# Kernel tuning notes

Measured on AMD Instinct MI355X. Metric: run time of the kernel, lower is better.

## Reference

```python
import jax, jax.numpy as jnp
import numpy as np

B, C, O, K, H, W = 32, 256, 256, 7, 31, 31


def _unfold(x, k):
    """Extract kxk sliding windows (stride 1, no padding, no dilation).

    x: [B, C, H, W] -> patches [B, C, k, k, Ho, Wo]
    """
    _, _, h, w = x.shape
    ho, wo = h - k + 1, w - k + 1
    # fixed small loop over k*k window offsets (k=7 -> 49 cheap slices)
    rows = []
    for i in range(k):
        cols = [x[:, :, i:i + ho, j:j + wo] for j in range(k)]
        rows.append(jnp.stack(cols, axis=2))  # [B, C, k, Ho, Wo]
    return jnp.stack(rows, axis=2)  # [B, C, k, k, Ho, Wo]


def setup_inputs() -> dict:
    key = jax.random.key(0)
    k1, k2, k3, k4 = jax.random.split(key, 4)
    x = jax.random.normal(k1, (B, C, H, W), dtype=jnp.float32)
    kernel = jax.random.normal(k2, (B, C, K, K), dtype=jnp.float32)
    weight = jax.random.normal(k3, (O, C, K, K), dtype=jnp.float32) * 0.02
    bias = jax.random.normal(k4, (O,), dtype=jnp.float32) * 0.02
    return {"x": x, "kernel": kernel, "weight": weight, "bias": bias}


def reference(x, kernel, weight, bias):
    k = weight.shape[-1]
    patches = _unfold(x, k)  # [B, C, k, k, Ho, Wo]
    # fused: (patches * kernel[..., None, None]) contracted with weight
    # torch: einsum('ijklmn,ojkl->iomn', patches * kernel_view, weight)
    out = jnp.einsum('bcklhw,bckl,ockl->bohw', patches, kernel, weight)
    out = out + bias[None, :, None, None]
    return out
```

## Files before the change

### kernel.cpp

```cpp
#include <hip/hip_runtime.h>
#include <hip/hip_bf16.h>

typedef __attribute__((ext_vector_type(8)))  short short8;
typedef __attribute__((ext_vector_type(4)))  float floatx4;
typedef __attribute__((ext_vector_type(16))) float floatx16;

#define BB 32
#define CC 256
#define OO 256
#define KS 7
#define HH 31
#define WW 31
#define HO 25
#define PP 625
#define SS 49

#define SLAB_PITCH 40
#define SLAB_ROWS  310

#define WT4_ELEMS  ((size_t)SS * 8 * 2 * CC * 16)
#define WT4_BYTES  (WT4_ELEMS * 2)
#define KERNF_BYTES ((size_t)BB * SS * CC * 4)
#define WMOD_ELEMS ((size_t)BB * WT4_ELEMS)
#define WMOD_BYTES (WMOD_ELEMS * 2)

static __device__ __forceinline__ unsigned pk2(float lo, float hi) {
    float2 f; f.x = lo; f.y = hi;
    __hip_bfloat162 h = __float22bfloat162_rn(f);
    unsigned r;
    __builtin_memcpy(&r, &h, sizeof(r));
    return r;
}
static __device__ __forceinline__ float bflo(unsigned u) {
    return __builtin_bit_cast(float, u << 16);
}
static __device__ __forceinline__ float bfhi(unsigned u) {
    return __builtin_bit_cast(float, u & 0xffff0000u);
}

static __device__ __forceinline__ uint4 modpack(uint4 wv, float4 k0, float4 k1) {
    float p0 = bflo(wv.x) * k0.x, p1 = bfhi(wv.x) * k0.y;
    float p2 = bflo(wv.y) * k0.z, p3 = bfhi(wv.y) * k0.w;
    float p4 = bflo(wv.z) * k1.x, p5 = bfhi(wv.z) * k1.y;
    float p6 = bflo(wv.w) * k1.z, p7 = bfhi(wv.w) * k1.w;
    uint4 r;
    r.x = pk2(p0, p1); r.y = pk2(p2, p3); r.z = pk2(p4, p5); r.w = pk2(p6, p7);
    return r;
}

__global__ __launch_bounds__(256) void repack_w(const float* __restrict__ w,
                                                unsigned short* __restrict__ wt4) {
    const int bid = blockIdx.x;
    const int s = bid >> 3, cb = bid & 7;
    const int o = threadIdx.x;
    const float* src = w + ((size_t)o * CC + cb * 32) * SS + s;
    float v[32];
#pragma unroll
    for (int ci = 0; ci < 32; ++ci) v[ci] = src[(size_t)ci * SS];
#pragma unroll
    for (int kh = 0; kh < 2; ++kh) {
        unsigned short* dst = wt4 + ((size_t)bid * 2 + kh) * (CC * 16) + o * 16;
        uint4 p0, p1;
        p0.x = pk2(v[kh*16+0], v[kh*16+1]);  p0.y = pk2(v[kh*16+2], v[kh*16+3]);
        p0.z = pk2(v[kh*16+4], v[kh*16+5]);  p0.w = pk2(v[kh*16+6], v[kh*16+7]);
        p1.x = pk2(v[kh*16+8], v[kh*16+9]);  p1.y = pk2(v[kh*16+10], v[kh*16+11]);
        p1.z = pk2(v[kh*16+12], v[kh*16+13]); p1.w = pk2(v[kh*16+14], v[kh*16+15]);
        *(uint4*)(dst)     = p0;
        *(uint4*)(dst + 8) = p1;
    }
}

__global__ __launch_bounds__(256) void repack_k(const float* __restrict__ kern,
                                                float* __restrict__ kernf) {
    const int bid = blockIdx.x;
    const int b = bid / KS, kk = bid % KS;
    const int c = threadIdx.x;
    const float* src = kern + ((size_t)b * CC + c) * SS + kk * KS;
#pragma unroll
    for (int ll = 0; ll < KS; ++ll)
        kernf[((size_t)b * SS + kk * KS + ll) * CC + c] = src[ll];
}

__global__ __launch_bounds__(256) void premod(
        const unsigned short* __restrict__ wt4, const float* __restrict__ kern,
        unsigned short* __restrict__ wmod) {
    const int bid = blockIdx.x;
    const int b = bid / 392, rc = bid % 392;
    const int s = rc >> 3, cb = rc & 7;
    const int o = threadIdx.x;
    const float* kp = kern + ((size_t)b * CC + cb * 32) * SS + s;
    float kf[32];
#pragma unroll
    for (int ci = 0; ci < 32; ++ci) kf[ci] = kp[(size_t)ci * SS];
#pragma unroll
    for (int kh = 0; kh < 2; ++kh) {
        const size_t off = ((size_t)rc * 2 + kh) * (CC * 16) + o * 16;
        uint4 w0 = *(const uint4*)(wt4 + off);
        uint4 w1 = *(const uint4*)(wt4 + off + 8);
        float4 k0a, k0b, k1a, k1b;
        k0a.x = kf[kh*16+0];  k0a.y = kf[kh*16+1];  k0a.z = kf[kh*16+2];  k0a.w = kf[kh*16+3];
        k0b.x = kf[kh*16+4];  k0b.y = kf[kh*16+5];  k0b.z = kf[kh*16+6];  k0b.w = kf[kh*16+7];
        k1a.x = kf[kh*16+8];  k1a.y = kf[kh*16+9];  k1a.z = kf[kh*16+10]; k1a.w = kf[kh*16+11];
        k1b.x = kf[kh*16+12]; k1b.y = kf[kh*16+13]; k1b.z = kf[kh*16+14]; k1b.w = kf[kh*16+15];
        uint4 m0 = modpack(w0, k0a, k0b);
        uint4 m1 = modpack(w1, k1a, k1b);
        unsigned short* dst = wmod + (size_t)b * WT4_ELEMS + off;
        *(uint4*)(dst)     = m0;
        *(uint4*)(dst + 8) = m1;
    }
}

__global__ __launch_bounds__(256, 4) void dwconv_big(
        const float* __restrict__ x, const unsigned short* __restrict__ wmod,
        const float* __restrict__ bias, float* __restrict__ out) {
    __shared__ unsigned short slab[SLAB_ROWS * SLAB_PITCH];

    const int tid = threadIdx.x;
    const int id = blockIdx.x;
    const int hi = id / 80, rem = id % 80;
    const int px = rem >> 3;
    const int g = hi * 8 + (rem & 7);
    const int b = g >> 2, oy = g & 3;

    const int p0 = px * 64, o0 = oy * 64;
    const int h0 = p0 / HO;
    const int pmax = (p0 + 63 < PP - 1) ? p0 + 63 : PP - 1;
    const int rows = pmax / HO - h0 + 7;
    const int npos = rows * WW;

    const int lane = tid & 63, kw = tid >> 6;
    const int l32 = lane & 31, half = lane >> 5;

    int bOff[2];
#pragma unroll
    for (int ph = 0; ph < 2; ++ph) {
        int p = p0 + ph * 32 + l32;
        if (p > PP - 1) p = PP - 1;
        int h = p / HO, ww_ = p - h * HO;
        bOff[ph] = ((h - h0) * WW + ww_) * SLAB_PITCH + half * 8;
    }

    const int s0 = kw * 12 + (kw > 0 ? 1 : 0);
    const int ns = kw ? 12 : 13;

    const unsigned short* wmodb = wmod + (size_t)b * WT4_ELEMS
                                  + (size_t)(o0 + l32) * 16 + half * 8;

    floatx16 acc[2][2];
#pragma unroll
    for (int oh = 0; oh < 2; ++oh)
#pragma unroll
        for (int ph = 0; ph < 2; ++ph)
#pragma unroll
            for (int r = 0; r < 16; ++r) acc[oh][ph][r] = 0.f;

    for (int cb = 0; cb < 8; ++cb) {
        __syncthreads();
        {
            const float* xsrc = x + ((size_t)(b * CC + cb * 32 + kw * 8)) * (HH * WW)
                                  + h0 * WW;
#pragma unroll
            for (int it = 0; it < 5; ++it) {
                int pos = lane + it * 64;
                if (pos < npos) {
                    float v[8];
#pragma unroll
                    for (int j = 0; j < 8; ++j) v[j] = xsrc[j * (HH * WW) + pos];
                    uint4 pkt;
                    pkt.x = pk2(v[0], v[1]); pkt.y = pk2(v[2], v[3]);
                    pkt.z = pk2(v[4], v[5]); pkt.w = pk2(v[6], v[7]);
                    *(uint4*)(slab + pos * SLAB_PITCH + kw * 8) = pkt;
                }
            }
        }
        __syncthreads();

        const unsigned short* aptr = wmodb + (size_t)(s0 * 8 + cb) * 8192;

        uint4 wa0 = *(const uint4*)(aptr);
        uint4 wa1 = *(const uint4*)(aptr + 512);
        uint4 wa2 = *(const uint4*)(aptr + 4096);
        uint4 wa3 = *(const uint4*)(aptr + 4096 + 512);

        int s = s0, kk = s0 / KS, ll = s0 - (s0 / KS) * KS;
        for (int si = 0; si < ns; ++si) {
            uint4 wn0, wn1, wn2, wn3;
            if (si + 1 < ns) {
                aptr += 65536;
                wn0 = *(const uint4*)(aptr);
                wn1 = *(const uint4*)(aptr + 512);
                wn2 = *(const uint4*)(aptr + 4096);
                wn3 = *(const uint4*)(aptr + 4096 + 512);
            } else {
                wn0 = wa0; wn1 = wa1; wn2 = wa2; wn3 = wa3;
            }

            const unsigned short* slabS = slab + (kk * WW + ll) * SLAB_PITCH;
            short8 sb00 = *(const short8*)(slabS + bOff[0]);
            short8 sb01 = *(const short8*)(slabS + bOff[0] + 16);
            short8 sb10 = *(const short8*)(slabS + bOff[1]);
            short8 sb11 = *(const short8*)(slabS + bOff[1] + 16);

            short8 a00 = __builtin_bit_cast(short8, wa0);
            short8 a10 = __builtin_bit_cast(short8, wa1);
            short8 a01 = __builtin_bit_cast(short8, wa2);
            short8 a11 = __builtin_bit_cast(short8, wa3);

            acc[0][0] = __builtin_amdgcn_mfma_f32_32x32x16_bf16(a00, sb00, acc[0][0], 0, 0, 0);
            acc[0][1] = __builtin_amdgcn_mfma_f32_32x32x16_bf16(a00, sb10, acc[0][1], 0, 0, 0);
            acc[1][0] = __builtin_amdgcn_mfma_f32_32x32x16_bf16(a10, sb00, acc[1][0], 0, 0, 0);
            acc[1][1] = __builtin_amdgcn_mfma_f32_32x32x16_bf16(a10, sb10, acc[1][1], 0, 0, 0);
            acc[0][0] = __builtin_amdgcn_mfma_f32_32x32x16_bf16(a01, sb01, acc[0][0], 0, 0, 0);
            acc[0][1] = __builtin_amdgcn_mfma_f32_32x32x16_bf16(a01, sb11, acc[0][1], 0, 0, 0);
            acc[1][0] = __builtin_amdgcn_mfma_f32_32x32x16_bf16(a11, sb01, acc[1][0], 0, 0, 0);
            acc[1][1] = __builtin_amdgcn_mfma_f32_32x32x16_bf16(a11, sb11, acc[1][1], 0, 0, 0);

            wa0 = wn0; wa1 = wn1; wa2 = wn2; wa3 = wn3;
            ++s; if (++ll == KS) { ll = 0; ++kk; }
        }
    }

    float* red = (float*)slab;
    __syncthreads();
    if (kw == 3) {
#pragma unroll
        for (int oh = 0; oh < 2; ++oh)
#pragma unroll
            for (int ph = 0; ph < 2; ++ph)
#pragma unroll
                for (int c = 0; c < 4; ++c) {
                    floatx4 v4 = {acc[oh][ph][4*c+0], acc[oh][ph][4*c+1],
                                  acc[oh][ph][4*c+2], acc[oh][ph][4*c+3]};
                    *(floatx4*)(red + (ph * 32 + l32) * 68 + oh * 32 + c * 8 + 4 * half) = v4;
                }
    }
    __syncthreads();
    if (kw == 2) {
#pragma unroll
        for (int oh = 0; oh < 2; ++oh)
#pragma unroll
            for (int ph = 0; ph < 2; ++ph)
#pragma unroll
                for (int c = 0; c < 4; ++c) {
                    float* rp = red + (ph * 32 + l32) * 68 + oh * 32 + c * 8 + 4 * half;
                    floatx4 v4 = *(floatx4*)rp;
                    v4[0] += acc[oh][ph][4*c+0]; v4[1] += acc[oh][ph][4*c+1];
                    v4[2] += acc[oh][ph][4*c+2]; v4[3] += acc[oh][ph][4*c+3];
                    *(floatx4*)rp = v4;
                }
    }
    __syncthreads();
    if (kw == 1) {
#pragma unroll
        for (int oh = 0; oh < 2; ++oh)
#pragma unroll
            for (int ph = 0; ph < 2; ++ph)
#pragma unroll
                for (int c = 0; c < 4; ++c) {
                    float* rp = red + (ph * 32 + l32) * 68 + oh * 32 + c * 8 + 4 * half;
                    floatx4 v4 = *(floatx4*)rp;
                    v4[0] += acc[oh][ph][4*c+0]; v4[1] += acc[oh][ph][4*c+1];
                    v4[2] += acc[oh][ph][4*c+2]; v4[3] += acc[oh][ph][4*c+3];
                    *(floatx4*)rp = v4;
                }
    }
    __syncthreads();
    if (kw == 0) {
#pragma unroll
        for (int oh = 0; oh < 2; ++oh)
#pragma unroll
            for (int c = 0; c < 4; ++c) {
                const int ob = o0 + oh * 32 + c * 8 + 4 * half;
                const float4 bv = *(const float4*)(bias + ob);
#pragma unroll
                for (int ph = 0; ph < 2; ++ph) {
                    const int p = p0 + ph * 32 + l32;
                    floatx4 v4 = *(floatx4*)(red + (ph * 32 + l32) * 68 + oh * 32 + c * 8 + 4 * half);
                    if (p < PP) {
                        out[((size_t)(b * OO + ob + 0)) * PP + p] = v4[0] + acc[oh][ph][4*c+0] + bv.x;
                        out[((size_t)(b * OO + ob + 1)) * PP + p] = v4[1] + acc[oh][ph][4*c+1] + bv.y;
                        out[((size_t)(b * OO + ob + 2)) * PP + p] = v4[2] + acc[oh][ph][4*c+2] + bv.z;
                        out[((size_t)(b * OO + ob + 3)) * PP + p] = v4[3] + acc[oh][ph][4*c+3] + bv.w;
                    }
                }
            }
    }
}

#define SLAB2_ROWS 372
__global__ __launch_bounds__(256, 3) void dwconv_mid(
        const float* __restrict__ x,
        const unsigned short* __restrict__ wt4, const float* __restrict__ kernf,
        const float* __restrict__ bias, float* __restrict__ out) {
    __shared__ unsigned short slab[SLAB2_ROWS * SLAB_PITCH];

    const int tid = threadIdx.x;
    const int id = blockIdx.x;
    const int oy = id & 3;
    const int t  = id >> 2;
    const int px = t % 5, b = t / 5;
    const int p0 = px * 128, o0 = oy * 64;
    const int h0 = p0 / HO;
    const int rows = (HH - h0) < 12 ? (HH - h0) : 12;
    const int npos = rows * WW;

    const int lane = tid & 63, wid = tid >> 6;
    const int pw = wid & 1, kw = wid >> 1;
    const int lo16 = lane & 15, quad = lane >> 4;

    int bOff[4];
#pragma unroll
    for (int pt = 0; pt < 4; ++pt) {
        int p = p0 + pw * 64 + pt * 16 + lo16;
        if (p > PP - 1) p = PP - 1;
        int h = p / HO, ww_ = p - h * HO;
        bOff[pt] = ((h - h0) * WW + ww_) * SLAB_PITCH + quad * 8;
    }

    const int s0 = kw ? 25 : 0;
    const int ns = kw ? 24 : 25;

    floatx4 acc[4][4];
#pragma unroll
    for (int at = 0; at < 4; ++at)
#pragma unroll
        for (int pt = 0; pt < 4; ++pt)
            acc[at][pt] = (floatx4){0.f, 0.f, 0.f, 0.f};

    for (int cb = 0; cb < 8; ++cb) {
        __syncthreads();
        {
            const int coct = wid;
            const float* xsrc = x + ((size_t)(b * CC + cb * 32 + coct * 8)) * (HH * WW)
                                  + h0 * WW;
#pragma unroll
            for (int it = 0; it < 6; ++it) {
                int pos = lane + it * 64;
                if (pos < npos) {
                    float v[8];
#pragma unroll
                    for (int j = 0; j < 8; ++j) v[j] = xsrc[j * (HH * WW) + pos];
                    uint4 pkt;
                    pkt.x = pk2(v[0], v[1]); pkt.y = pk2(v[2], v[3]);
                    pkt.z = pk2(v[4], v[5]); pkt.w = pk2(v[6], v[7]);
                    *(uint4*)(slab + pos * SLAB_PITCH + coct * 8) = pkt;
                }
            }
        }
        __syncthreads();

        const unsigned short* aptrA = wt4 +
            ((size_t)(s0 * 8 + cb) * 2 + (quad >> 1)) * 4096 +
            (size_t)(o0 + lo16) * 16 + (quad & 1) * 8;
        const float* kptr = kernf + ((size_t)b * SS + s0) * CC + cb * 32 + quad * 8;

        uint4 wa[4];
        wa[0] = *(const uint4*)(aptrA);
        wa[1] = *(const uint4*)(aptrA + 256);
        wa[2] = *(const uint4*)(aptrA + 512);
        wa[3] = *(const uint4*)(aptrA + 768);
        float4 kq0 = *(const float4*)(kptr);
        float4 kq1 = *(const float4*)(kptr + 4);

        for (int si = 0; si < ns; ++si) {
            const int s = s0 + si;
            uint4 wn[4]; float4 kn0, kn1;
            if (si + 1 < ns) {
                aptrA += 65536;
                kptr  += CC;
                wn[0] = *(const uint4*)(aptrA);
                wn[1] = *(const uint4*)(aptrA + 256);
                wn[2] = *(const uint4*)(aptrA + 512);
                wn[3] = *(const uint4*)(aptrA + 768);
                kn0 = *(const float4*)(kptr);
                kn1 = *(const float4*)(kptr + 4);
            } else {
                wn[0] = wa[0]; wn[1] = wa[1]; wn[2] = wa[2]; wn[3] = wa[3];
                kn0 = kq0; kn1 = kq1;
            }

            const int kk = s / KS, ll = s - kk * KS;
            const unsigned short* slabS = slab + (kk * WW + ll) * SLAB_PITCH;

            short8 sb0 = *(const short8*)(slabS + bOff[0]);
            short8 sb1 = *(const short8*)(slabS + bOff[1]);
            short8 sb2 = *(const short8*)(slabS + bOff[2]);
            short8 sb3 = *(const short8*)(slabS + bOff[3]);

            short8 sa0 = __builtin_bit_cast(short8, modpack(wa[0], kq0, kq1));
            short8 sa1 = __builtin_bit_cast(short8, modpack(wa[1], kq0, kq1));
            short8 sa2 = __builtin_bit_cast(short8, modpack(wa[2], kq0, kq1));
            short8 sa3 = __builtin_bit_cast(short8, modpack(wa[3], kq0, kq1));

            acc[0][0] = __builtin_amdgcn_mfma_f32_16x16x32_bf16(sa0, sb0, acc[0][0], 0, 0, 0);
            acc[0][1] = __builtin_amdgcn_mfma_f32_16x16x32_bf16(sa0, sb1, acc[0][1], 0, 0, 0);
            acc[0][2] = __builtin_amdgcn_mfma_f32_16x16x32_bf16(sa0, sb2, acc[0][2], 0, 0, 0);
            acc[0][3] = __builtin_amdgcn_mfma_f32_16x16x32_bf16(sa0, sb3, acc[0][3], 0, 0, 0);
            acc[1][0] = __builtin_amdgcn_mfma_f32_16x16x32_bf16(sa1, sb0, acc[1][0], 0, 0, 0);
            acc[1][1] = __builtin_amdgcn_mfma_f32_16x16x32_bf16(sa1, sb1, acc[1][1], 0, 0, 0);
            acc[1][2] = __builtin_amdgcn_mfma_f32_16x16x32_bf16(sa1, sb2, acc[1][2], 0, 0, 0);
            acc[1][3] = __builtin_amdgcn_mfma_f32_16x16x32_bf16(sa1, sb3, acc[1][3], 0, 0, 0);
            acc[2][0] = __builtin_amdgcn_mfma_f32_16x16x32_bf16(sa2, sb0, acc[2][0], 0, 0, 0);
            acc[2][1] = __builtin_amdgcn_mfma_f32_16x16x32_bf16(sa2, sb1, acc[2][1], 0, 0, 0);
            acc[2][2] = __builtin_amdgcn_mfma_f32_16x16x32_bf16(sa2, sb2, acc[2][2], 0, 0, 0);
            acc[2][3] = __builtin_amdgcn_mfma_f32_16x16x32_bf16(sa2, sb3, acc[2][3], 0, 0, 0);
            acc[3][0] = __builtin_amdgcn_mfma_f32_16x16x32_bf16(sa3, sb0, acc[3][0], 0, 0, 0);
            acc[3][1] = __builtin_amdgcn_mfma_f32_16x16x32_bf16(sa3, sb1, acc[3][1], 0, 0, 0);
            acc[3][2] = __builtin_amdgcn_mfma_f32_16x16x32_bf16(sa3, sb2, acc[3][2], 0, 0, 0);
            acc[3][3] = __builtin_amdgcn_mfma_f32_16x16x32_bf16(sa3, sb3, acc[3][3], 0, 0, 0);

            wa[0] = wn[0]; wa[1] = wn[1]; wa[2] = wn[2]; wa[3] = wn[3];
            kq0 = kn0; kq1 = kn1;
        }
    }

    float* red = (float*)slab;
    for (int round = 0; round < 2; ++round) {
        __syncthreads();
        if (kw == 1 && pw == round) {
#pragma unroll
            for (int at = 0; at < 4; ++at)
#pragma unroll
                for (int pt = 0; pt < 4; ++pt)
                    *(floatx4*)(red + (pt * 16 + lo16) * 68 + at * 16 + quad * 4)
                        = acc[at][pt];
        }
        __syncthreads();
        if (kw == 0 && pw == round) {
#pragma unroll
            for (int at = 0; at < 4; ++at) {
                const float4 bv = *(const float4*)(bias + o0 + at * 16 + quad * 4);
#pragma unroll
                for (int pt = 0; pt < 4; ++pt) {
                    floatx4 v = *(const floatx4*)(red + (pt * 16 + lo16) * 68
                                                  + at * 16 + quad * 4);
                    int p = p0 + round * 64 + pt * 16 + lo16;
                    if (p < PP) {
                        const int ob = o0 + at * 16 + quad * 4;
                        out[((size_t)(b * OO + ob + 0)) * PP + p] = acc[at][pt][0] + v[0] + bv.x;
                        out[((size_t)(b * OO + ob + 1)) * PP + p] = acc[at][pt][1] + v[1] + bv.y;
                        out[((size_t)(b * OO + ob + 2)) * PP + p] = acc[at][pt][2] + v[2] + bv.z;
                        out[((size_t)(b * OO + ob + 3)) * PP + p] = acc[at][pt][3] + v[3] + bv.w;
                    }
                }
            }
        }
    }
}

__global__ __launch_bounds__(256) void dwconv_naive(
        const float* __restrict__ x, const float* __restrict__ kern,
        const float* __restrict__ w, const float* __restrict__ bias,
        float* __restrict__ out) {
    const int idx = blockIdx.x * 256 + threadIdx.x;
    if (idx >= BB * OO * PP) return;
    const int p = idx % PP;
    const int o = (idx / PP) % OO;
    const int b = idx / (PP * OO);
    const int h = p / HO;
    const int wq = p - h * HO;
    float acc = 0.f;
    for (int c = 0; c < CC; ++c) {
        const float* xp = x + ((size_t)(b * CC + c)) * (HH * WW) + h * WW + wq;
        const float* kp = kern + ((size_t)b * CC + c) * SS;
        const float* wp = w + ((size_t)o * CC + c) * SS;
#pragma unroll
        for (int s = 0; s < SS; ++s) {
            const int kk = s / KS;
            const int ll = s - kk * KS;
            acc += xp[kk * WW + ll] * kp[s] * wp[s];
        }
    }
    out[idx] = acc + bias[o];
}

extern "C" void kernel_launch(void* const* d_in, const int* in_sizes, int n_in,
                              void* d_out, int out_size, void* d_ws, size_t ws_size,
                              hipStream_t stream) {
    const float* x    = (const float*)d_in[0];
    const float* kern = (const float*)d_in[1];
    const float* w    = (const float*)d_in[2];
    const float* bias = (const float*)d_in[3];
    float* out = (float*)d_out;

    if (ws_size >= WT4_BYTES + WMOD_BYTES) {
        unsigned short* wt4  = (unsigned short*)d_ws;
        unsigned short* wmod = (unsigned short*)((char*)d_ws + WT4_BYTES);
        repack_w<<<dim3(SS * 8), dim3(256), 0, stream>>>(w, wt4);
        premod<<<dim3(BB * SS * 8), dim3(256), 0, stream>>>(wt4, kern, wmod);
        dwconv_big<<<dim3(1280), dim3(256), 0, stream>>>(x, wmod, bias, out);
    } else if (ws_size >= WT4_BYTES + KERNF_BYTES) {
        unsigned short* wt4 = (unsigned short*)d_ws;
        float* kernf = (float*)((char*)d_ws + WT4_BYTES);
        repack_w<<<dim3(SS * 8), dim3(256), 0, stream>>>(w, wt4);
        repack_k<<<dim3(BB * KS), dim3(256), 0, stream>>>(kern, kernf);
        dwconv_mid<<<dim3(640), dim3(256), 0, stream>>>(x, wt4, kernf, bias, out);
    } else {
        const int total = BB * OO * PP;
        dwconv_naive<<<dim3((total + 255) / 256), dim3(256), 0, stream>>>(
            x, kern, w, bias, out);
    }
}
```

Measured before the change: 304.3 us.

## Fuse per-batch weight modulation into conv kernel, drop premodulated weight buffer

Removes the premod pass, which wrote a per-batch bf16 copy of the modulated weights (tens of MB), and applies the kernel modulation inside the conv loop. Each block now stages the 32x49 kernel slice in LDS per channel block. The block is also retiled: each wave owns 32 outputs across all 49 taps for 96 positions, so the cross-wave LDS reduction disappears. In exchange the kernel does more VALU modulation work per MFMA and runs a smaller grid of 448 blocks at lower occupancy.

```diff
diff --git a/kernel.cpp b/kernel.cpp
--- a/kernel.cpp
+++ b/kernel.cpp
@@ -16,13 +16,13 @@
 #define SS 49
 
 #define SLAB_PITCH 40
-#define SLAB_ROWS  310
+#define SLAB_ROWS  341
+#define P_TILE 96
+#define NPX 7
+#define KP 36
 
 #define WT4_ELEMS  ((size_t)SS * 8 * 2 * CC * 16)
 #define WT4_BYTES  (WT4_ELEMS * 2)
-#define KERNF_BYTES ((size_t)BB * SS * CC * 4)
-#define WMOD_ELEMS ((size_t)BB * WT4_ELEMS)
-#define WMOD_BYTES (WMOD_ELEMS * 2)
 
 static __device__ __forceinline__ unsigned pk2(float lo, float hi) {
     float2 f; f.x = lo; f.y = hi;
@@ -70,97 +70,54 @@
     }
 }
 
-__global__ __launch_bounds__(256) void repack_k(const float* __restrict__ kern,
-                                                float* __restrict__ kernf) {
-    const int bid = blockIdx.x;
-    const int b = bid / KS, kk = bid % KS;
-    const int c = threadIdx.x;
-    const float* src = kern + ((size_t)b * CC + c) * SS + kk * KS;
-#pragma unroll
-    for (int ll = 0; ll < KS; ++ll)
-        kernf[((size_t)b * SS + kk * KS + ll) * CC + c] = src[ll];
-}
-
-__global__ __launch_bounds__(256) void premod(
-        const unsigned short* __restrict__ wt4, const float* __restrict__ kern,
-        unsigned short* __restrict__ wmod) {
-    const int bid = blockIdx.x;
-    const int b = bid / 392, rc = bid % 392;
-    const int s = rc >> 3, cb = rc & 7;
-    const int o = threadIdx.x;
-    const float* kp = kern + ((size_t)b * CC + cb * 32) * SS + s;
-    float kf[32];
-#pragma unroll
-    for (int ci = 0; ci < 32; ++ci) kf[ci] = kp[(size_t)ci * SS];
-#pragma unroll
-    for (int kh = 0; kh < 2; ++kh) {
-        const size_t off = ((size_t)rc * 2 + kh) * (CC * 16) + o * 16;
-        uint4 w0 = *(const uint4*)(wt4 + off);
-        uint4 w1 = *(const uint4*)(wt4 + off + 8);
-        float4 k0a, k0b, k1a, k1b;
-        k0a.x = kf[kh*16+0];  k0a.y = kf[kh*16+1];  k0a.z = kf[kh*16+2];  k0a.w = kf[kh*16+3];
-        k0b.x = kf[kh*16+4];  k0b.y = kf[kh*16+5];  k0b.z = kf[kh*16+6];  k0b.w = kf[kh*16+7];
-        k1a.x = kf[kh*16+8];  k1a.y = kf[kh*16+9];  k1a.z = kf[kh*16+10]; k1a.w = kf[kh*16+11];
-        k1b.x = kf[kh*16+12]; k1b.y = kf[kh*16+13]; k1b.z = kf[kh*16+14]; k1b.w = kf[kh*16+15];
-        uint4 m0 = modpack(w0, k0a, k0b);
-        uint4 m1 = modpack(w1, k1a, k1b);
-        unsigned short* dst = wmod + (size_t)b * WT4_ELEMS + off;
-        *(uint4*)(dst)     = m0;
-        *(uint4*)(dst + 8) = m1;
-    }
-}
-
-__global__ __launch_bounds__(256, 4) void dwconv_big(
-        const float* __restrict__ x, const unsigned short* __restrict__ wmod,
-        const float* __restrict__ bias, float* __restrict__ out) {
+__global__ __launch_bounds__(256, 3) void dwconv_fused(
+        const float* __restrict__ x, const unsigned short* __restrict__ wt4,
+        const float* __restrict__ kern, const float* __restrict__ bias,
+        float* __restrict__ out) {
     __shared__ unsigned short slab[SLAB_ROWS * SLAB_PITCH];
+    __shared__ float klds[SS * KP];
 
     const int tid = threadIdx.x;
     const int id = blockIdx.x;
-    const int hi = id / 80, rem = id % 80;
-    const int px = rem >> 3;
-    const int g = hi * 8 + (rem & 7);
-    const int b = g >> 2, oy = g & 3;
-
-    const int p0 = px * 64, o0 = oy * 64;
+    const int q = id >> 3, r = id & 7;
+    const int oy = r >> 2;
+    const int m = q * 4 + (r & 3);
+    const int b = m / NPX, px = m - (m / NPX) * NPX;
+
+    const int p0 = px * P_TILE;
     const int h0 = p0 / HO;
-    const int pmax = (p0 + 63 < PP - 1) ? p0 + 63 : PP - 1;
+    const int pmax = (p0 + P_TILE - 1 < PP - 1) ? p0 + P_TILE - 1 : PP - 1;
     const int rows = pmax / HO - h0 + 7;
     const int npos = rows * WW;
 
-    const int lane = tid & 63, kw = tid >> 6;
+    const int lane = tid & 63, wid = tid >> 6;
     const int l32 = lane & 31, half = lane >> 5;
 
-    int bOff[2];
-#pragma unroll
-    for (int ph = 0; ph < 2; ++ph) {
+    int bOff[3];
+#pragma unroll
+    for (int ph = 0; ph < 3; ++ph) {
         int p = p0 + ph * 32 + l32;
         if (p > PP - 1) p = PP - 1;
         int h = p / HO, ww_ = p - h * HO;
         bOff[ph] = ((h - h0) * WW + ww_) * SLAB_PITCH + half * 8;
     }
 
-    const int s0 = kw * 12 + (kw > 0 ? 1 : 0);
-    const int ns = kw ? 12 : 13;
-
-    const unsigned short* wmodb = wmod + (size_t)b * WT4_ELEMS
-                                  + (size_t)(o0 + l32) * 16 + half * 8;
-
-    floatx16 acc[2][2];
-#pragma unroll
-    for (int oh = 0; oh < 2; ++oh)
-#pragma unroll
-        for (int ph = 0; ph < 2; ++ph)
-#pragma unroll
-            for (int r = 0; r < 16; ++r) acc[oh][ph][r] = 0.f;
+    const unsigned short* wbase = wt4
+        + (size_t)(oy * 128 + wid * 32 + l32) * 16 + half * 8;
+
+    floatx16 acc[3];
+#pragma unroll
+    for (int ph = 0; ph < 3; ++ph)
+#pragma unroll
+        for (int rr = 0; rr < 16; ++rr) acc[ph][rr] = 0.f;
 
     for (int cb = 0; cb < 8; ++cb) {
         __syncthreads();
         {
-            const float* xsrc = x + ((size_t)(b * CC + cb * 32 + kw * 8)) * (HH * WW)
+            const float* xsrc = x + ((size_t)(b * CC + cb * 32 + wid * 8)) * (HH * WW)
                                   + h0 * WW;
 #pragma unroll
-            for (int it = 0; it < 5; ++it) {
+            for (int it = 0; it < 6; ++it) {
                 int pos = lane + it * 64;
                 if (pos < npos) {
                     float v[8];
@@ -169,280 +126,81 @@
                     uint4 pkt;
                     pkt.x = pk2(v[0], v[1]); pkt.y = pk2(v[2], v[3]);
                     pkt.z = pk2(v[4], v[5]); pkt.w = pk2(v[6], v[7]);
-                    *(uint4*)(slab + pos * SLAB_PITCH + kw * 8) = pkt;
+                    *(uint4*)(slab + pos * SLAB_PITCH + wid * 8) = pkt;
                 }
             }
         }
+        {
+            const float* ksrc = kern + ((size_t)(b * CC + cb * 32)) * SS;
+#pragma unroll
+            for (int it = 0; it < 7; ++it) {
+                int f = tid + it * 256;
+                if (f < 32 * SS) {
+                    int c = f / SS, s = f - c * SS;
+                    klds[s * KP + c] = ksrc[f];
+                }
+            }
+        }
         __syncthreads();
 
-        const unsigned short* aptr = wmodb + (size_t)(s0 * 8 + cb) * 8192;
+        const unsigned short* aptr = wbase + (size_t)cb * 8192;
 
         uint4 wa0 = *(const uint4*)(aptr);
-        uint4 wa1 = *(const uint4*)(aptr + 512);
-        uint4 wa2 = *(const uint4*)(aptr + 4096);
-        uint4 wa3 = *(const uint4*)(aptr + 4096 + 512);
-
-        int s = s0, kk = s0 / KS, ll = s0 - (s0 / KS) * KS;
-        for (int si = 0; si < ns; ++si) {
-            uint4 wn0, wn1, wn2, wn3;
-            if (si + 1 < ns) {
+        uint4 wa1 = *(const uint4*)(aptr + 4096);
+
+        int kk = 0, ll = 0;
+        for (int si = 0; si < SS; ++si) {
+            uint4 wn0, wn1;
+            if (si + 1 < SS) {
                 aptr += 65536;
                 wn0 = *(const uint4*)(aptr);
-                wn1 = *(const uint4*)(aptr + 512);
-                wn2 = *(const uint4*)(aptr + 4096);
-                wn3 = *(const uint4*)(aptr + 4096 + 512);
+                wn1 = *(const uint4*)(aptr + 4096);
             } else {
-                wn0 = wa0; wn1 = wa1; wn2 = wa2; wn3 = wa3;
-            }
+                wn0 = wa0; wn1 = wa1;
+            }
+
+            const float* kp = klds + si * KP;
+            float4 k0a = *(const float4*)(kp + half * 8);
+            float4 k0b = *(const float4*)(kp + half * 8 + 4);
+            float4 k1a = *(const float4*)(kp + 16 + half * 8);
+            float4 k1b = *(const float4*)(kp + 16 + half * 8 + 4);
 
             const unsigned short* slabS = slab + (kk * WW + ll) * SLAB_PITCH;
             short8 sb00 = *(const short8*)(slabS + bOff[0]);
             short8 sb01 = *(const short8*)(slabS + bOff[0] + 16);
             short8 sb10 = *(const short8*)(slabS + bOff[1]);
             short8 sb11 = *(const short8*)(slabS + bOff[1] + 16);
-
-            short8 a00 = __builtin_bit_cast(short8, wa0);
-            short8 a10 = __builtin_bit_cast(short8, wa1);
-            short8 a01 = __builtin_bit_cast(short8, wa2);
-            short8 a11 = __builtin_bit_cast(short8, wa3);
-
-            acc[0][0] = __builtin_amdgcn_mfma_f32_32x32x16_bf16(a00, sb00, acc[0][0], 0, 0, 0);
-            acc[0][1] = __builtin_amdgcn_mfma_f32_32x32x16_bf16(a00, sb10, acc[0][1], 0, 0, 0);
-            acc[1][0] = __builtin_amdgcn_mfma_f32_32x32x16_bf16(a10, sb00, acc[1][0], 0, 0, 0);
-            acc[1][1] = __builtin_amdgcn_mfma_f32_32x32x16_bf16(a10, sb10, acc[1][1], 0, 0, 0);
-            acc[0][0] = __builtin_amdgcn_mfma_f32_32x32x16_bf16(a01, sb01, acc[0][0], 0, 0, 0);
-            acc[0][1] = __builtin_amdgcn_mfma_f32_32x32x16_bf16(a01, sb11, acc[0][1], 0, 0, 0);
-            acc[1][0] = __builtin_amdgcn_mfma_f32_32x32x16_bf16(a11, sb01, acc[1][0], 0, 0, 0);
-            acc[1][1] = __builtin_amdgcn_mfma_f32_32x32x16_bf16(a11, sb11, acc[1][1], 0, 0, 0);
-
-            wa0 = wn0; wa1 = wn1; wa2 = wn2; wa3 = wn3;
-            ++s; if (++ll == KS) { ll = 0; ++kk; }
-        }
-    }
-
-    float* red = (float*)slab;
-    __syncthreads();
-    if (kw == 3) {
-#pragma unroll
-        for (int oh = 0; oh < 2; ++oh)
-#pragma unroll
-            for (int ph = 0; ph < 2; ++ph)
-#pragma unroll
-                for (int c = 0; c < 4; ++c) {
-                    floatx4 v4 = {acc[oh][ph][4*c+0], acc[oh][ph][4*c+1],
-                                  acc[oh][ph][4*c+2], acc[oh][ph][4*c+3]};
-                    *(floatx4*)(red + (ph * 32 + l32) * 68 + oh * 32 + c * 8 + 4 * half) = v4;
-                }
-    }
-    __syncthreads();
-    if (kw == 2) {
-#pragma unroll
-        for (int oh = 0; oh < 2; ++oh)
-#pragma unroll
-            for (int ph = 0; ph < 2; ++ph)
-#pragma unroll
-                for (int c = 0; c < 4; ++c) {
-                    float* rp = red + (ph * 32 + l32) * 68 + oh * 32 + c * 8 + 4 * half;
-                    floatx4 v4 = *(floatx4*)rp;
-                    v4[0] += acc[oh][ph][4*c+0]; v4[1] += acc[oh][ph][4*c+1];
-                    v4[2] += acc[oh][ph][4*c+2]; v4[3] += acc[oh][ph][4*c+3];
-                    *(floatx4*)rp = v4;
-                }
-    }
-    __syncthreads();
-    if (kw == 1) {
-#pragma unroll
-        for (int oh = 0; oh < 2; ++oh)
-#pragma unroll
-            for (int ph = 0; ph < 2; ++ph)
-#pragma unroll
-                for (int c = 0; c < 4; ++c) {
-                    float* rp = red + (ph * 32 + l32) * 68 + oh * 32 + c * 8 + 4 * half;
-                    floatx4 v4 = *(floatx4*)rp;
-                    v4[0] += acc[oh][ph][4*c+0]; v4[1] += acc[oh][ph][4*c+1];
-                    v4[2] += acc[oh][ph][4*c+2]; v4[3] += acc[oh][ph][4*c+3];
-                    *(floatx4*)rp = v4;
-                }
-    }
-    __syncthreads();
-    if (kw == 0) {
-#pragma unroll
-        for (int oh = 0; oh < 2; ++oh)
-#pragma unroll
-            for (int c = 0; c < 4; ++c) {
-                const int ob = o0 + oh * 32 + c * 8 + 4 * half;
-                const float4 bv = *(const float4*)(bias + ob);
-#pragma unroll
-                for (int ph = 0; ph < 2; ++ph) {
-                    const int p = p0 + ph * 32 + l32;
-                    floatx4 v4 = *(floatx4*)(red + (ph * 32 + l32) * 68 + oh * 32 + c * 8 + 4 * half);
-                    if (p < PP) {
-                        out[((size_t)(b * OO + ob + 0)) * PP + p] = v4[0] + acc[oh][ph][4*c+0] + bv.x;
-                        out[((size_t)(b * OO + ob + 1)) * PP + p] = v4[1] + acc[oh][ph][4*c+1] + bv.y;
-                        out[((size_t)(b * OO + ob + 2)) * PP + p] = v4[2] + acc[oh][ph][4*c+2] + bv.z;
-                        out[((size_t)(b * OO + ob + 3)) * PP + p] = v4[3] + acc[oh][ph][4*c+3] + bv.w;
-                    }
-                }
-            }
-    }
-}
-
-#define SLAB2_ROWS 372
-__global__ __launch_bounds__(256, 3) void dwconv_mid(
-        const float* __restrict__ x,
-        const unsigned short* __restrict__ wt4, const float* __restrict__ kernf,
-        const float* __restrict__ bias, float* __restrict__ out) {
-    __shared__ unsigned short slab[SLAB2_ROWS * SLAB_PITCH];
-
-    const int tid = threadIdx.x;
-    const int id = blockIdx.x;
-    const int oy = id & 3;
-    const int t  = id >> 2;
-    const int px = t % 5, b = t / 5;
-    const int p0 = px * 128, o0 = oy * 64;
-    const int h0 = p0 / HO;
-    const int rows = (HH - h0) < 12 ? (HH - h0) : 12;
-    const int npos = rows * WW;
-
-    const int lane = tid & 63, wid = tid >> 6;
-    const int pw = wid & 1, kw = wid >> 1;
-    const int lo16 = lane & 15, quad = lane >> 4;
-
-    int bOff[4];
-#pragma unroll
-    for (int pt = 0; pt < 4; ++pt) {
-        int p = p0 + pw * 64 + pt * 16 + lo16;
-        if (p > PP - 1) p = PP - 1;
-        int h = p / HO, ww_ = p - h * HO;
-        bOff[pt] = ((h - h0) * WW + ww_) * SLAB_PITCH + quad * 8;
-    }
-
-    const int s0 = kw ? 25 : 0;
-    const int ns = kw ? 24 : 25;
-
-    floatx4 acc[4][4];
-#pragma unroll
-    for (int at = 0; at < 4; ++at)
-#pragma unroll
-        for (int pt = 0; pt < 4; ++pt)
-            acc[at][pt] = (floatx4){0.f, 0.f, 0.f, 0.f};
-
-    for (int cb = 0; cb < 8; ++cb) {
-        __syncthreads();
-        {
-            const int coct = wid;
-            const float* xsrc = x + ((size_t)(b * CC + cb * 32 + coct * 8)) * (HH * WW)
-                                  + h0 * WW;
-#pragma unroll
-            for (int it = 0; it < 6; ++it) {
-                int pos = lane + it * 64;
-                if (pos < npos) {
-                    float v[8];
-#pragma unroll
-                    for (int j = 0; j < 8; ++j) v[j] = xsrc[j * (HH * WW) + pos];
-                    uint4 pkt;
-                    pkt.x = pk2(v[0], v[1]); pkt.y = pk2(v[2], v[3]);
-                    pkt.z = pk2(v[4], v[5]); pkt.w = pk2(v[6], v[7]);
-                    *(uint4*)(slab + pos * SLAB_PITCH + coct * 8) = pkt;
-                }
-            }
-        }
-        __syncthreads();
-
-        const unsigned short* aptrA = wt4 +
-            ((size_t)(s0 * 8 + cb) * 2 + (quad >> 1)) * 4096 +
-            (size_t)(o0 + lo16) * 16 + (quad & 1) * 8;
-        const float* kptr = kernf + ((size_t)b * SS + s0) * CC + cb * 32 + quad * 8;
-
-        uint4 wa[4];
-        wa[0] = *(const uint4*)(aptrA);
-        wa[1] = *(const uint4*)(aptrA + 256);
-        wa[2] = *(const uint4*)(aptrA + 512);
-        wa[3] = *(const uint4*)(aptrA + 768);
-        float4 kq0 = *(const float4*)(kptr);
-        float4 kq1 = *(const float4*)(kptr + 4);
-
-        for (int si = 0; si < ns; ++si) {
-            const int s = s0 + si;
-            uint4 wn[4]; float4 kn0, kn1;
-            if (si + 1 < ns) {
-                aptrA += 65536;
-                kptr  += CC;
-                wn[0] = *(const uint4*)(aptrA);
-                wn[1] = *(const uint4*)(aptrA + 256);
-                wn[2] = *(const uint4*)(aptrA + 512);
-                wn[3] = *(const uint4*)(aptrA + 768);
-                kn0 = *(const float4*)(kptr);
-                kn1 = *(const float4*)(kptr + 4);
-            } else {
-                wn[0] = wa[0]; wn[1] = wa[1]; wn[2] = wa[2]; wn[3] = wa[3];
-                kn0 = kq0; kn1 = kq1;
-            }
-
-            const int kk = s / KS, ll = s - kk * KS;
-            const unsigned short* slabS = slab + (kk * WW + ll) * SLAB_PITCH;
-
-            short8 sb0 = *(const short8*)(slabS + bOff[0]);
-            short8 sb1 = *(const short8*)(slabS + bOff[1]);
-            short8 sb2 = *(const short8*)(slabS + bOff[2]);
-            short8 sb3 = *(const short8*)(slabS + bOff[3]);
-
-            short8 sa0 = __builtin_bit_cast(short8, modpack(wa[0], kq0, kq1));
-            short8 sa1 = __builtin_bit_cast(short8, modpack(wa[1], kq0, kq1));
-            short8 sa2 = __builtin_bit_cast(short8, modpack(wa[2], kq0, kq1));
-            short8 sa3 = __builtin_bit_cast(short8, modpack(wa[3], kq0, kq1));
-
-            acc[0][0] = __builtin_amdgcn_mfma_f32_16x16x32_bf16(sa0, sb0, acc[0][0], 0, 0, 0);
-            acc[0][1] = __builtin_amdgcn_mfma_f32_16x16x32_bf16(sa0, sb1, acc[0][1], 0, 0, 0);
-            acc[0][2] = __builtin_amdgcn_mfma_f32_16x16x32_bf16(sa0, sb2, acc[0][2], 0, 0, 0);
-            acc[0][3] = __builtin_amdgcn_mfma_f32_16x16x32_bf16(sa0, sb3, acc[0][3], 0, 0, 0);
-            acc[1][0] = __builtin_amdgcn_mfma_f32_16x16x32_bf16(sa1, sb0, acc[1][0], 0, 0, 0);
-            acc[1][1] = __builtin_amdgcn_mfma_f32_16x16x32_bf16(sa1, sb1, acc[1][1], 0, 0, 0);
-            acc[1][2] = __builtin_amdgcn_mfma_f32_16x16x32_bf16(sa1, sb2, acc[1][2], 0, 0, 0);
-            acc[1][3] = __builtin_amdgcn_mfma_f32_16x16x32_bf16(sa1, sb3, acc[1][3], 0, 0, 0);
-            acc[2][0] = __builtin_amdgcn_mfma_f32_16x16x32_bf16(sa2, sb0, acc[2][0], 0, 0, 0);
-            acc[2][1] = __builtin_amdgcn_mfma_f32_16x16x32_bf16(sa2, sb1, acc[2][1], 0, 0, 0);
-            acc[2][2] = __builtin_amdgcn_mfma_f32_16x16x32_bf16(sa2, sb2, acc[2][2], 0, 0, 0);
-            acc[2][3] = __builtin_amdgcn_mfma_f32_16x16x32_bf16(sa2, sb3, acc[2][3], 0, 0, 0);
-            acc[3][0] = __builtin_amdgcn_mfma_f32_16x16x32_bf16(sa3, sb0, acc[3][0], 0, 0, 0);
-            acc[3][1] = __builtin_amdgcn_mfma_f32_16x16x32_bf16(sa3, sb1, acc[3][1], 0, 0, 0);
-            acc[3][2] = __builtin_amdgcn_mfma_f32_16x16x32_bf16(sa3, sb2, acc[3][2], 0, 0, 0);
-            acc[3][3] = __builtin_amdgcn_mfma_f32_16x16x32_bf16(sa3, sb3, acc[3][3], 0, 0, 0);
-
-            wa[0] = wn[0]; wa[1] = wn[1]; wa[2] = wn[2]; wa[3] = wn[3];
-            kq0 = kn0; kq1 = kn1;
-        }
-    }
-
-    float* red = (float*)slab;
-    for (int round = 0; round < 2; ++round) {
-        __syncthreads();
-        if (kw == 1 && pw == round) {
-#pragma unroll
-            for (int at = 0; at < 4; ++at)
-#pragma unroll
-                for (int pt = 0; pt < 4; ++pt)
-                    *(floatx4*)(red + (pt * 16 + lo16) * 68 + at * 16 + quad * 4)
-                        = acc[at][pt];
-        }
-        __syncthreads();
-        if (kw == 0 && pw == round) {
-#pragma unroll
-            for (int at = 0; at < 4; ++at) {
-                const float4 bv = *(const float4*)(bias + o0 + at * 16 + quad * 4);
-#pragma unroll
-                for (int pt = 0; pt < 4; ++pt) {
-                    floatx4 v = *(const floatx4*)(red + (pt * 16 + lo16) * 68
-                                                  + at * 16 + quad * 4);
-                    int p = p0 + round * 64 + pt * 16 + lo16;
-                    if (p < PP) {
-                        const int ob = o0 + at * 16 + quad * 4;
-                        out[((size_t)(b * OO + ob + 0)) * PP + p] = acc[at][pt][0] + v[0] + bv.x;
-                        out[((size_t)(b * OO + ob + 1)) * PP + p] = acc[at][pt][1] + v[1] + bv.y;
-                        out[((size_t)(b * OO + ob + 2)) * PP + p] = acc[at][pt][2] + v[2] + bv.z;
-                        out[((size_t)(b * OO + ob + 3)) * PP + p] = acc[at][pt][3] + v[3] + bv.w;
-                    }
-                }
+            short8 sb20 = *(const short8*)(slabS + bOff[2]);
+            short8 sb21 = *(const short8*)(slabS + bOff[2] + 16);
+
+            short8 a0 = __builtin_bit_cast(short8, modpack(wa0, k0a, k0b));
+            short8 a1 = __builtin_bit_cast(short8, modpack(wa1, k1a, k1b));
+
+            acc[0] = __builtin_amdgcn_mfma_f32_32x32x16_bf16(a0, sb00, acc[0], 0, 0, 0);
+            acc[1] = __builtin_amdgcn_mfma_f32_32x32x16_bf16(a0, sb10, acc[1], 0, 0, 0);
+            acc[2] = __builtin_amdgcn_mfma_f32_32x32x16_bf16(a0, sb20, acc[2], 0, 0, 0);
+            acc[0] = __builtin_amdgcn_mfma_f32_32x32x16_bf16(a1, sb01, acc[0], 0, 0, 0);
+            acc[1] = __builtin_amdgcn_mfma_f32_32x32x16_bf16(a1, sb11, acc[1], 0, 0, 0);
+            acc[2] = __builtin_amdgcn_mfma_f32_32x32x16_bf16(a1, sb21, acc[2], 0, 0, 0);
+
+            wa0 = wn0; wa1 = wn1;
+            if (++ll == KS) { ll = 0; ++kk; }
+        }
+    }
+
+    const int ow0 = oy * 128 + wid * 32;
+#pragma unroll
+    for (int c = 0; c < 4; ++c) {
+        const int ob = ow0 + c * 8 + 4 * half;
+        const float4 bv = *(const float4*)(bias + ob);
+#pragma unroll
+        for (int ph = 0; ph < 3; ++ph) {
+            const int p = p0 + ph * 32 + l32;
+            if (p < PP) {
+                out[((size_t)(b * OO + ob + 0)) * PP + p] = acc[ph][4*c+0] + bv.x;
+                out[((size_t)(b * OO + ob + 1)) * PP + p] = acc[ph][4*c+1] + bv.y;
+                out[((size_t)(b * OO + ob + 2)) * PP + p] = acc[ph][4*c+2] + bv.z;
+                out[((size_t)(b * OO + ob + 3)) * PP + p] = acc[ph][4*c+3] + bv.w;
             }
         }
     }
@@ -483,18 +241,10 @@
     const float* bias = (const float*)d_in[3];
     float* out = (float*)d_out;
 
-    if (ws_size >= WT4_BYTES + WMOD_BYTES) {
-        unsigned short* wt4  = (unsigned short*)d_ws;
-        unsigned short* wmod = (unsigned short*)((char*)d_ws + WT4_BYTES);
+    if (ws_size >= WT4_BYTES) {
+        unsigned short* wt4 = (unsigned short*)d_ws;
         repack_w<<<dim3(SS * 8), dim3(256), 0, stream>>>(w, wt4);
-        premod<<<dim3(BB * SS * 8), dim3(256), 0, stream>>>(wt4, kern, wmod);
-        dwconv_big<<<dim3(1280), dim3(256), 0, stream>>>(x, wmod, bias, out);
-    } else if (ws_size >= WT4_BYTES + KERNF_BYTES) {
-        unsigned short* wt4 = (unsigned short*)d_ws;
-        float* kernf = (float*)((char*)d_ws + WT4_BYTES);
-        repack_w<<<dim3(SS * 8), dim3(256), 0, stream>>>(w, wt4);
-        repack_k<<<dim3(BB * KS), dim3(256), 0, stream>>>(kern, kernf);
-        dwconv_mid<<<dim3(640), dim3(256), 0, stream>>>(x, wt4, kernf, bias, out);
+        dwconv_fused<<<dim3(448), dim3(256), 0, stream>>>(x, wt4, kern, bias, out);
     } else {
         const int total = BB * OO * PP;
         dwconv_naive<<<dim3((total + 255) / 256), dim3(256), 0, stream>>>(
```

Measured after the change: 321.3 us. 1.06x slower.
